# Kernel tuning notes

Hardware: AMD Instinct MI355X
Metric: run time of the kernel (lower is better)

The kernel has to match this reference:

```python
import jax, jax.numpy as jnp
import numpy as np

EMBED = 1024
HEADS = 16
HEAD_DIM = EMBED // HEADS
LN_EPS = 1e-5


def setup_inputs() -> dict:
    key = jax.random.key(0)
    ks = jax.random.split(key, 12)
    B, LQ, LK = 2, 2048, 2048
    s = 1.0 / np.sqrt(EMBED)
    inp = {
        "query_seq": jax.random.normal(ks[0], (B, LQ, EMBED), jnp.float32),
        "key_value_seq": jax.random.normal(ks[1], (B, LK, EMBED), jnp.float32),
        "prompt_size": 0,
        "Wq": jax.random.normal(ks[2], (EMBED, EMBED), jnp.float32) * s,
        "bq": jnp.zeros((EMBED,), jnp.float32),
        "Wk": jax.random.normal(ks[3], (EMBED, EMBED), jnp.float32) * s,
        "bk": jnp.zeros((EMBED,), jnp.float32),
        "Wv": jax.random.normal(ks[4], (EMBED, EMBED), jnp.float32) * s,
        "bv": jnp.zeros((EMBED,), jnp.float32),
        "Wo": jax.random.normal(ks[5], (EMBED, EMBED), jnp.float32) * s,
        "bo": jnp.zeros((EMBED,), jnp.float32),
        "ln_gamma": jnp.ones((EMBED,), jnp.float32),
        "ln_beta": jnp.zeros((EMBED,), jnp.float32),
    }
    return inp


def _split_heads(x):
    B, L, _ = x.shape
    return x.reshape(B, L, HEADS, HEAD_DIM).transpose(0, 2, 1, 3)  # [B,H,L,Dh]


def reference(query_seq, key_value_seq, prompt_size, Wq, bq, Wk, bk, Wv, bv, Wo, bo, ln_gamma, ln_beta):
    # projections (torch nn.Linear: x @ W.T + b)
    q = _split_heads(query_seq @ Wq.T + bq)
    k = _split_heads(key_value_seq @ Wk.T + bk)
    v = _split_heads(key_value_seq @ Wv.T + bv)
    # naive attention: full score matrix, softmax over keys
    scores = jnp.einsum("bhqd,bhkd->bhqk", q, k) / np.sqrt(HEAD_DIM).astype(np.float32)
    attn = jax.nn.softmax(scores, axis=-1)
    ctx = jnp.einsum("bhqk,bhkd->bhqd", attn, v)
    B, H, LQ, Dh = ctx.shape
    ctx = ctx.transpose(0, 2, 1, 3).reshape(B, LQ, H * Dh)
    out = ctx @ Wo.T + bo
    # residual + LayerNorm
    x = out + query_seq
    mu = jnp.mean(x, axis=-1, keepdims=True)
    var = jnp.var(x, axis=-1, keepdims=True)
    return (x - mu) * jax.lax.rsqrt(var + LN_EPS) * ln_gamma + ln_beta
```

## Files before the change

kernel.cpp:

```cpp
#include <hip/hip_runtime.h>

typedef unsigned short u16;
typedef unsigned int u32;
typedef __attribute__((ext_vector_type(8))) __bf16 bf16x8;
typedef __attribute__((ext_vector_type(4))) float f32x4;
typedef __attribute__((ext_vector_type(16))) float f32x16;

#define EMBED 1024
#define NB 2
#define LQ 2048
#define HEADS 16
#define DH 64
#define QSCALE 0.18033688011112042f

__device__ __forceinline__ u16 f2bf(float f) {
  u32 u = __float_as_uint(f);
  u32 r = (u + 0x7FFFu + ((u >> 16) & 1u)) >> 16;
  return (u16)r;
}

__device__ __forceinline__ void glds16(const void* g, void* l) {
  __builtin_amdgcn_global_load_lds((const __attribute__((address_space(1))) void*)g,
                                   (__attribute__((address_space(3))) void*)l, 16, 0, 0);
}

__device__ __forceinline__ f32x4 mfma16(bf16x8 a, bf16x8 b, f32x4 c) {
  return __builtin_amdgcn_mfma_f32_16x16x32_bf16(a, b, c, 0, 0, 0);
}
__device__ __forceinline__ f32x16 mfma32(bf16x8 a, bf16x8 b, f32x16 c) {
  return __builtin_amdgcn_mfma_f32_32x32x16_bf16(a, b, c, 0, 0, 0);
}

__device__ __forceinline__ void pl32(u32& a, u32& b) {
  asm("v_permlane32_swap_b32 %0, %1" : "+v"(a), "+v"(b));
}

__device__ __forceinline__ u32 packbf(float a, float b) {
  return __builtin_amdgcn_perm(__float_as_uint(b), __float_as_uint(a), 0x07060302u);
}

__global__ __launch_bounds__(256) void cast_kernel(
    const float* __restrict__ q, const float* __restrict__ kv,
    const float* __restrict__ wq, const float* __restrict__ wk,
    const float* __restrict__ wv, const float* __restrict__ wo,
    u16* __restrict__ qb, u16* __restrict__ kvb, u16* __restrict__ wqb,
    u16* __restrict__ wkb, u16* __restrict__ wvb, u16* __restrict__ wob) {
  int bid = blockIdx.x;
  const float* src;
  u16* dst;
  long base;
  if (bid < 2048) {
    src = q; dst = qb; base = (long)bid * 2048;
  } else if (bid < 4096) {
    src = kv; dst = kvb; base = (long)(bid - 2048) * 2048;
  } else {
    int wsel = (bid - 4096) >> 9;
    int wb = (bid - 4096) & 511;
    if (wsel == 0) { src = wq; dst = wqb; }
    else if (wsel == 1) { src = wk; dst = wkb; }
    else if (wsel == 2) { src = wv; dst = wvb; }
    else { src = wo; dst = wob; }
    base = (long)wb * 2048;
  }
  long e = base + (long)threadIdx.x * 8;
  float4 f0 = *(const float4*)(src + e);
  float4 f1 = *(const float4*)(src + e + 4);
  uint4 o;
  o.x = (u32)f2bf(f0.x) | ((u32)f2bf(f0.y) << 16);
  o.y = (u32)f2bf(f0.z) | ((u32)f2bf(f0.w) << 16);
  o.z = (u32)f2bf(f1.x) | ((u32)f2bf(f1.y) << 16);
  o.w = (u32)f2bf(f1.z) | ((u32)f2bf(f1.w) << 16);
  *(uint4*)(dst + e) = o;
}

template <int IT>
__device__ __forceinline__ void gemm_core(
    u16* As, u16* Bs, const u16* __restrict__ A, const u16* __restrict__ W,
    const float* __restrict__ bias, const float* __restrict__ resid,
    void* __restrict__ outp, int mode, int bx, int by) {
  const int K = EMBED;
  const int TM = IT * 32;
  const int tid = threadIdx.x;
  const int lane = tid & 63;
  const int wv = tid >> 6;
  const int wm = wv >> 1, wn = wv & 1;
  const int l16 = lane & 15, quad = lane >> 4;
  const long tile_m = (long)bx * TM;
  const long tile_n = (long)by * 128;

  f32x4 z4 = {0.f, 0.f, 0.f, 0.f};
  f32x4 acc[IT][4];
#pragma unroll
  for (int i = 0; i < IT; i++)
#pragma unroll
    for (int j = 0; j < 4; j++) acc[i][j] = z4;

  for (int k0 = 0; k0 < K; k0 += 64) {
#pragma unroll
    for (int it = 0; it < TM / 32; it++) {
      int lin = it * 256 + tid;
      int row = lin >> 3, cc = lin & 7;
      glds16(A + (tile_m + row) * K + k0 + ((cc ^ (row & 7)) << 3), As + lin * 8);
    }
#pragma unroll
    for (int it = 0; it < 4; it++) {
      int lin = it * 256 + tid;
      int row = lin >> 3, cc = lin & 7;
      glds16(W + (tile_n + row) * K + k0 + ((cc ^ (row & 7)) << 3), Bs + lin * 8);
    }
    __syncthreads();
#pragma unroll
    for (int ki = 0; ki < 2; ki++) {
      bf16x8 af[IT], bfr[4];
#pragma unroll
      for (int i = 0; i < IT; i++) {
        int row = wm * (IT * 16) + i * 16 + l16;
        af[i] = *(const bf16x8*)(As + row * 64 + (((ki * 4 + quad) ^ (row & 7)) << 3));
      }
#pragma unroll
      for (int j = 0; j < 4; j++) {
        int row = wn * 64 + j * 16 + l16;
        bfr[j] = *(const bf16x8*)(Bs + row * 64 + (((ki * 4 + quad) ^ (row & 7)) << 3));
      }
#pragma unroll
      for (int i = 0; i < IT; i++)
#pragma unroll
        for (int j = 0; j < 4; j++) acc[i][j] = mfma16(af[i], bfr[j], acc[i][j]);
    }
    __syncthreads();
  }

#pragma unroll
  for (int j = 0; j < 4; j++) {
    int gn = (int)tile_n + wn * 64 + j * 16 + l16;
    float bv = bias[gn];
#pragma unroll
    for (int i = 0; i < IT; i++) {
      long gm0 = tile_m + wm * (IT * 16) + i * 16 + quad * 4;
      if (mode == 3) {
#pragma unroll
        for (int r = 0; r < 4; r++) {
          long idx = (gm0 + r) * EMBED + gn;
          ((float*)outp)[idx] = acc[i][j][r] + bv + resid[idx];
        }
      } else if (mode == 2) {
        int b = (int)(gm0 >> 11), l = (int)(gm0 & 2047);
        int hh = gn >> 6, dh = gn & 63;
        uint2 pk;
        pk.x = (u32)f2bf(acc[i][j][0] + bv) | ((u32)f2bf(acc[i][j][1] + bv) << 16);
        pk.y = (u32)f2bf(acc[i][j][2] + bv) | ((u32)f2bf(acc[i][j][3] + bv) << 16);
        *(uint2*)((u16*)outp + (long)((b * HEADS + hh) * DH + dh) * LQ + l) = pk;
      } else {
#pragma unroll
        for (int r = 0; r < 4; r++) {
          long gm = gm0 + r;
          float v = acc[i][j][r] + bv;
          if (mode == 0) v *= QSCALE;
          int b = (int)(gm >> 11), l = (int)(gm & 2047);
          int hh = gn >> 6, dh = gn & 63;
          ((u16*)outp)[(long)((b * HEADS + hh) * LQ + l) * DH + dh] = f2bf(v);
        }
      }
    }
  }
}

__device__ __forceinline__ void xcd_map(int id, int& bx, int& by) {
  int xcd = id & 7, j = id >> 3;
  bx = (xcd << 3) | (j & 7);
  by = j >> 3;
}

__global__ __launch_bounds__(256, 4) void qkv_kernel(
    const u16* __restrict__ qb, const u16* __restrict__ kvb,
    const u16* __restrict__ wqb, const u16* __restrict__ wkb, const u16* __restrict__ wvb,
    const float* __restrict__ bq, const float* __restrict__ bk, const float* __restrict__ bv,
    u16* __restrict__ Qh, u16* __restrict__ Kh, u16* __restrict__ Vt) {
  __shared__ u16 As[64 * 64];
  __shared__ u16 Bs[128 * 64];
  int bx, by;
  xcd_map((int)blockIdx.x, bx, by);
  int z = blockIdx.y;
  if (z == 0)      gemm_core<2>(As, Bs, qb,  wqb, bq, nullptr, Qh, 0, bx, by);
  else if (z == 1) gemm_core<2>(As, Bs, kvb, wkb, bk, nullptr, Kh, 1, bx, by);
  else             gemm_core<2>(As, Bs, kvb, wvb, bv, nullptr, Vt, 2, bx, by);
}

__global__ __launch_bounds__(256, 4) void oproj_kernel(
    const u16* __restrict__ ctx, const u16* __restrict__ wob,
    const float* __restrict__ bo, const float* __restrict__ resid, float* __restrict__ out) {
  __shared__ u16 As[64 * 64];
  __shared__ u16 Bs[128 * 64];
  int bx, by;
  xcd_map((int)blockIdx.x, bx, by);
  gemm_core<2>(As, Bs, ctx, wob, bo, resid, out, 3, bx, by);
}

__global__ __launch_bounds__(512, 4) void attn_kernel(
    const u16* __restrict__ Qh, const u16* __restrict__ Kh,
    const u16* __restrict__ Vt, u16* __restrict__ ctx) {
  __shared__ u16 KVs[4][2][64 * 64];
  const int tid = threadIdx.x;
  const int lane = tid & 63;
  const int wv = tid >> 6;
  const int qsub = wv >> 1;
  const int kh = wv & 1;
  const int l32 = lane & 31, h = lane >> 5;
  const int bid = (int)blockIdx.x;
  const int swz = (bid & 7) * 64 + (bid >> 3);
  const int bh = swz >> 4, qt = swz & 15;
  const long qoff = (long)bh * (LQ * DH) + (long)qt * (128 * DH);
  const long koff = (long)bh * (LQ * DH);
  const long voff = (long)bh * (DH * LQ);
  const int qbase = qsub * 32;
  const int krow = kh * 32 + l32;

#define STAGE_KV(t, N)                                                          \
  do {                                                                          \
    int row = tid >> 3, cc = tid & 7;                                           \
    glds16(Kh + koff + (long)((t) * 64 + row) * 64 + ((cc ^ (row & 7)) << 3),   \
           &KVs[N][0][0] + tid * 8);                                            \
    glds16(Vt + voff + (long)row * LQ + (t) * 64 + ((cc ^ (row & 7)) << 3),     \
           &KVs[N][1][0] + tid * 8);                                            \
  } while (0)

#define SYNC(W)                                                                 \
  do {                                                                          \
    asm volatile("s_waitcnt vmcnt(" #W ")" ::: "memory");                       \
    __builtin_amdgcn_s_barrier();                                               \
    asm volatile("" ::: "memory");                                              \
  } while (0)

  bf16x8 bq[4];
  {
    const u16* qp = Qh + qoff + (qbase + l32) * 64 + h * 8;
#pragma unroll
    for (int ks = 0; ks < 4; ks++) bq[ks] = *(const bf16x8*)(qp + ks * 16);
  }

  STAGE_KV(0, 0);
  STAGE_KV(1, 1);
  STAGE_KV(2, 2);
  SYNC(2);

  f32x16 z16 = {0.f, 0.f, 0.f, 0.f, 0.f, 0.f, 0.f, 0.f,
                0.f, 0.f, 0.f, 0.f, 0.f, 0.f, 0.f, 0.f};
  f32x16 ot[2];
  ot[0] = z16;
  ot[1] = z16;
  f32x16 st;
  uint2 pk[4];
  float2 ls2 = {0.f, 0.f};

#define DO_S(C)                                                                  \
  do {                                                                           \
    __builtin_amdgcn_s_setprio(1);                                               \
    _Pragma("unroll") for (int ks = 0; ks < 4; ks++) {                           \
      bf16x8 ak = *(const bf16x8*)(&KVs[C][0][0] + krow * 64 +                   \
                                   (((ks * 2 + h) ^ (krow & 7)) << 3));          \
      st = mfma32(ak, bq[ks], (ks == 0) ? z16 : st);                             \
    }                                                                            \
    __builtin_amdgcn_s_setprio(0);                                               \
  } while (0)

#define DO_SM()                                                                  \
  do {                                                                           \
    _Pragma("unroll") for (int g = 0; g < 4; g++) {                              \
      float p0 = __builtin_amdgcn_exp2f(st[g * 4 + 0]);                          \
      float p1 = __builtin_amdgcn_exp2f(st[g * 4 + 1]);                          \
      float p2 = __builtin_amdgcn_exp2f(st[g * 4 + 2]);                          \
      float p3 = __builtin_amdgcn_exp2f(st[g * 4 + 3]);                          \
      ls2.x += p0 + p2;                                                          \
      ls2.y += p1 + p3;                                                          \
      pk[g].x = packbf(p0, p1);                                                  \
      pk[g].y = packbf(p2, p3);                                                  \
    }                                                                            \
  } while (0)

#define DO_PV(P)                                                                 \
  do {                                                                           \
    _Pragma("unroll") for (int s = 0; s < 2; s++) {                              \
      uint2 wa = pk[s * 2];                                                      \
      uint2 wb = pk[s * 2 + 1];                                                  \
      u32 a0 = wa.x, b0 = wb.x, a1 = wa.y, b1 = wb.y;                            \
      pl32(a0, b0);                                                              \
      pl32(a1, b1);                                                              \
      union { u32 u[4]; bf16x8 v; } bp;                                          \
      bp.u[0] = a0;                                                              \
      bp.u[1] = a1;                                                              \
      bp.u[2] = b0;                                                              \
      bp.u[3] = b1;                                                              \
      __builtin_amdgcn_s_setprio(1);                                             \
      _Pragma("unroll") for (int mt2 = 0; mt2 < 2; mt2++) {                      \
        int row = mt2 * 32 + l32;                                                \
        int c = ((2 * kh + s) << 1) + h;                                         \
        bf16x8 av = *(const bf16x8*)(&KVs[P][1][0] + row * 64 +                  \
                                     ((c ^ (row & 7)) << 3));                    \
        ot[mt2] = mfma32(av, bp.v, ot[mt2]);                                     \
      }                                                                          \
      __builtin_amdgcn_s_setprio(0);                                             \
    }                                                                            \
  } while (0)

#define AITER(kt, P, C, N, W)                                                    \
  do {                                                                           \
    if ((kt) + 2 < 32) STAGE_KV((kt) + 2, N);                                    \
    DO_SM();                                                                     \
    DO_S(C);                                                                     \
    DO_PV(P);                                                                    \
    SYNC(W);                                                                     \
  } while (0)

  DO_S(0);

  AITER(1, 0, 1, 3, 2);
  for (int k0 = 2; k0 < 30; k0 += 4) {
    AITER(k0 + 0, 1, 2, 0, 2);
    AITER(k0 + 1, 2, 3, 1, 2);
    AITER(k0 + 2, 3, 0, 2, 2);
    AITER(k0 + 3, 0, 1, 3, 2);
  }
  AITER(30, 1, 2, 0, 0);
  AITER(31, 2, 3, 1, 0);
  DO_SM();
  DO_PV(3);

#undef STAGE_KV
#undef SYNC
#undef DO_S
#undef DO_SM
#undef DO_PV
#undef AITER

  float lsum = ls2.x + ls2.y;
  lsum += __shfl_xor(lsum, 32);

  float* mrgf = (float*)(&KVs[0][0][0]);
  float* mlsf = mrgf + 4 * 64 * 36;
  __syncthreads();
  if (kh == 1) {
    int mbase = (qsub * 64 + lane) * 36;
#pragma unroll
    for (int mt2 = 0; mt2 < 2; mt2++)
#pragma unroll
      for (int e = 0; e < 16; e++) mrgf[mbase + mt2 * 16 + e] = ot[mt2][e];
    mlsf[qsub * 64 + lane] = lsum;
  }
  __syncthreads();
  if (kh == 0) {
    int mbase = (qsub * 64 + lane) * 36;
    lsum += mlsf[qsub * 64 + lane];
    float inv = 1.0f / lsum;
    const int b = bh >> 4, head = bh & 15;
    int qrow = qt * 128 + qbase + l32;
    long base = (long)(b * LQ + qrow) * EMBED + head * DH;
#pragma unroll
    for (int mt2 = 0; mt2 < 2; mt2++) {
#pragma unroll
      for (int g = 0; g < 4; g++) {
        float o0 = (ot[mt2][g * 4 + 0] + mrgf[mbase + mt2 * 16 + g * 4 + 0]) * inv;
        float o1 = (ot[mt2][g * 4 + 1] + mrgf[mbase + mt2 * 16 + g * 4 + 1]) * inv;
        float o2 = (ot[mt2][g * 4 + 2] + mrgf[mbase + mt2 * 16 + g * 4 + 2]) * inv;
        float o3 = (ot[mt2][g * 4 + 3] + mrgf[mbase + mt2 * 16 + g * 4 + 3]) * inv;
        uint2 pkk;
        pkk.x = (u32)f2bf(o0) | ((u32)f2bf(o1) << 16);
        pkk.y = (u32)f2bf(o2) | ((u32)f2bf(o3) << 16);
        *(uint2*)(ctx + base + mt2 * 32 + g * 8 + 4 * h) = pkk;
      }
    }
  }
}

__global__ __launch_bounds__(256) void ln_kernel(
    float* __restrict__ x, const float* __restrict__ gamma, const float* __restrict__ beta) {
  const int lane = threadIdx.x & 63;
  const int wid = threadIdx.x >> 6;
  const long row = (long)blockIdx.x * 4 + wid;
  float* xr = x + row * EMBED;
  float4 v[4];
  float s = 0.f, sq = 0.f;
#pragma unroll
  for (int k = 0; k < 4; k++) {
    v[k] = *(const float4*)(xr + k * 256 + lane * 4);
    s += v[k].x + v[k].y + v[k].z + v[k].w;
    sq += v[k].x * v[k].x + v[k].y * v[k].y + v[k].z * v[k].z + v[k].w * v[k].w;
  }
#pragma unroll
  for (int off = 1; off < 64; off <<= 1) {
    s += __shfl_xor(s, off);
    sq += __shfl_xor(sq, off);
  }
  float mu = s * (1.f / EMBED);
  float var = sq * (1.f / EMBED) - mu * mu;
  float rstd = rsqrtf(var + 1e-5f);
#pragma unroll
  for (int k = 0; k < 4; k++) {
    float4 g = *(const float4*)(gamma + k * 256 + lane * 4);
    float4 bt = *(const float4*)(beta + k * 256 + lane * 4);
    float4 ov;
    ov.x = (v[k].x - mu) * rstd * g.x + bt.x;
    ov.y = (v[k].y - mu) * rstd * g.y + bt.y;
    ov.z = (v[k].z - mu) * rstd * g.z + bt.z;
    ov.w = (v[k].w - mu) * rstd * g.w + bt.w;
    *(float4*)(xr + k * 256 + lane * 4) = ov;
  }
}

extern "C" void kernel_launch(void* const* d_in, const int* in_sizes, int n_in,
                              void* d_out, int out_size, void* d_ws, size_t ws_size,
                              hipStream_t stream) {
  const float* q     = (const float*)d_in[0];
  const float* kv    = (const float*)d_in[1];
  const float* Wq    = (const float*)d_in[3];
  const float* bq    = (const float*)d_in[4];
  const float* Wk    = (const float*)d_in[5];
  const float* bk    = (const float*)d_in[6];
  const float* Wv    = (const float*)d_in[7];
  const float* bv    = (const float*)d_in[8];
  const float* Wo    = (const float*)d_in[9];
  const float* bo    = (const float*)d_in[10];
  const float* gamma = (const float*)d_in[11];
  const float* beta  = (const float*)d_in[12];

  char* ws = (char*)d_ws;
  u16* qb  = (u16*)(ws + (0l  << 20));
  u16* kvb = (u16*)(ws + (8l  << 20));
  u16* wqb = (u16*)(ws + (16l << 20));
  u16* wkb = (u16*)(ws + (18l << 20));
  u16* wvb = (u16*)(ws + (20l << 20));
  u16* wob = (u16*)(ws + (22l << 20));
  u16* Qh  = (u16*)(ws + (24l << 20));
  u16* Kh  = (u16*)(ws + (32l << 20));
  u16* Vt  = (u16*)(ws + (40l << 20));
  u16* ctx = (u16*)(ws + (48l << 20));
  float* out = (float*)d_out;

  cast_kernel<<<6144, 256, 0, stream>>>(q, kv, Wq, Wk, Wv, Wo, qb, kvb, wqb, wkb, wvb, wob);
  qkv_kernel<<<dim3(512, 3), 256, 0, stream>>>(qb, kvb, wqb, wkb, wvb, bq, bk, bv, Qh, Kh, Vt);
  attn_kernel<<<512, 512, 0, stream>>>(Qh, Kh, Vt, ctx);
  oproj_kernel<<<512, 256, 0, stream>>>(ctx, wob, bo, q, out);
  ln_kernel<<<1024, 256, 0, stream>>>(out, gamma, beta);
}
```

Measured before the change: 207.5 us.

## Fuse K and V projections into one GEMM block sharing the A tile

Adds a kv_core routine that computes the K and V projections together in each block. It loads the key/value activation tile once into LDS and reuses it against both Wk and Wv tiles, which halves the A-operand traffic for those two GEMMs. The qkv launch drops from 3 to 2 grid rows. In exchange, each block needs twice the B-tile LDS and twice the accumulator registers, and the kernel becomes imbalanced: the K/V blocks do double the work of the Q blocks.

New measurement: 203.4 us. 1.02x faster.

```diff
diff --git a/kernel.cpp b/kernel.cpp
--- a/kernel.cpp
+++ b/kernel.cpp
@@ -165,6 +165,100 @@
   }
 }
 
+__device__ __forceinline__ void kv_core(
+    u16* As, u16* Bk, u16* Bv,
+    const u16* __restrict__ A, const u16* __restrict__ Wk, const u16* __restrict__ Wv,
+    const float* __restrict__ bkb, const float* __restrict__ bvb,
+    u16* __restrict__ Kh, u16* __restrict__ Vt, int bx, int by) {
+  const int K = EMBED;
+  const int tid = threadIdx.x;
+  const int lane = tid & 63;
+  const int wvv = tid >> 6;
+  const int wm = wvv >> 1, wn = wvv & 1;
+  const int l16 = lane & 15, quad = lane >> 4;
+  const long tile_m = (long)bx * 64;
+  const long tile_n = (long)by * 128;
+
+  f32x4 z4 = {0.f, 0.f, 0.f, 0.f};
+  f32x4 accK[2][4], accV[2][4];
+#pragma unroll
+  for (int i = 0; i < 2; i++)
+#pragma unroll
+    for (int j = 0; j < 4; j++) { accK[i][j] = z4; accV[i][j] = z4; }
+
+  for (int k0 = 0; k0 < K; k0 += 64) {
+#pragma unroll
+    for (int it = 0; it < 2; it++) {
+      int lin = it * 256 + tid;
+      int row = lin >> 3, cc = lin & 7;
+      glds16(A + (tile_m + row) * K + k0 + ((cc ^ (row & 7)) << 3), As + lin * 8);
+    }
+#pragma unroll
+    for (int it = 0; it < 4; it++) {
+      int lin = it * 256 + tid;
+      int row = lin >> 3, cc = lin & 7;
+      glds16(Wk + (tile_n + row) * K + k0 + ((cc ^ (row & 7)) << 3), Bk + lin * 8);
+      glds16(Wv + (tile_n + row) * K + k0 + ((cc ^ (row & 7)) << 3), Bv + lin * 8);
+    }
+    __syncthreads();
+#pragma unroll
+    for (int ki = 0; ki < 2; ki++) {
+      bf16x8 af[2];
+#pragma unroll
+      for (int i = 0; i < 2; i++) {
+        int row = wm * 32 + i * 16 + l16;
+        af[i] = *(const bf16x8*)(As + row * 64 + (((ki * 4 + quad) ^ (row & 7)) << 3));
+      }
+      {
+        bf16x8 bf[4];
+#pragma unroll
+        for (int j = 0; j < 4; j++) {
+          int row = wn * 64 + j * 16 + l16;
+          bf[j] = *(const bf16x8*)(Bk + row * 64 + (((ki * 4 + quad) ^ (row & 7)) << 3));
+        }
+#pragma unroll
+        for (int i = 0; i < 2; i++)
+#pragma unroll
+          for (int j = 0; j < 4; j++) accK[i][j] = mfma16(af[i], bf[j], accK[i][j]);
+      }
+      {
+        bf16x8 bf[4];
+#pragma unroll
+        for (int j = 0; j < 4; j++) {
+          int row = wn * 64 + j * 16 + l16;
+          bf[j] = *(const bf16x8*)(Bv + row * 64 + (((ki * 4 + quad) ^ (row & 7)) << 3));
+        }
+#pragma unroll
+        for (int i = 0; i < 2; i++)
+#pragma unroll
+          for (int j = 0; j < 4; j++) accV[i][j] = mfma16(af[i], bf[j], accV[i][j]);
+      }
+    }
+    __syncthreads();
+  }
+
+#pragma unroll
+  for (int j = 0; j < 4; j++) {
+    int gn = (int)tile_n + wn * 64 + j * 16 + l16;
+    float bK = bkb[gn];
+    float bV = bvb[gn];
+    int hh = gn >> 6, dh = gn & 63;
+#pragma unroll
+    for (int i = 0; i < 2; i++) {
+      long gm0 = tile_m + wm * 32 + i * 16 + quad * 4;
+      int b = (int)(gm0 >> 11), l0 = (int)(gm0 & 2047);
+#pragma unroll
+      for (int r = 0; r < 4; r++) {
+        Kh[(long)((b * HEADS + hh) * LQ + (l0 + r)) * DH + dh] = f2bf(accK[i][j][r] + bK);
+      }
+      uint2 pk;
+      pk.x = (u32)f2bf(accV[i][j][0] + bV) | ((u32)f2bf(accV[i][j][1] + bV) << 16);
+      pk.y = (u32)f2bf(accV[i][j][2] + bV) | ((u32)f2bf(accV[i][j][3] + bV) << 16);
+      *(uint2*)(Vt + (long)((b * HEADS + hh) * DH + dh) * LQ + l0) = pk;
+    }
+  }
+}
+
 __device__ __forceinline__ void xcd_map(int id, int& bx, int& by) {
   int xcd = id & 7, j = id >> 3;
   bx = (xcd << 3) | (j & 7);
@@ -177,13 +271,13 @@
     const float* __restrict__ bq, const float* __restrict__ bk, const float* __restrict__ bv,
     u16* __restrict__ Qh, u16* __restrict__ Kh, u16* __restrict__ Vt) {
   __shared__ u16 As[64 * 64];
-  __shared__ u16 Bs[128 * 64];
+  __shared__ u16 Bs[2][128 * 64];
   int bx, by;
   xcd_map((int)blockIdx.x, bx, by);
-  int z = blockIdx.y;
-  if (z == 0)      gemm_core<2>(As, Bs, qb,  wqb, bq, nullptr, Qh, 0, bx, by);
-  else if (z == 1) gemm_core<2>(As, Bs, kvb, wkb, bk, nullptr, Kh, 1, bx, by);
-  else             gemm_core<2>(As, Bs, kvb, wvb, bv, nullptr, Vt, 2, bx, by);
+  if (blockIdx.y == 0)
+    gemm_core<2>(As, Bs[0], qb, wqb, bq, nullptr, Qh, 0, bx, by);
+  else
+    kv_core(As, Bs[0], Bs[1], kvb, wkb, wvb, bk, bv, Kh, Vt, bx, by);
 }
 
 __global__ __launch_bounds__(256, 4) void oproj_kernel(
@@ -436,7 +530,7 @@
   float* out = (float*)d_out;
 
   cast_kernel<<<6144, 256, 0, stream>>>(q, kv, Wq, Wk, Wv, Wo, qb, kvb, wqb, wkb, wvb, wob);
-  qkv_kernel<<<dim3(512, 3), 256, 0, stream>>>(qb, kvb, wqb, wkb, wvb, bq, bk, bv, Qh, Kh, Vt);
+  qkv_kernel<<<dim3(512, 2), 256, 0, stream>>>(qb, kvb, wqb, wkb, wvb, bq, bk, bv, Qh, Kh, Vt);
   attn_kernel<<<512, 512, 0, stream>>>(Qh, Kh, Vt, ctx);
   oproj_kernel<<<512, 256, 0, stream>>>(ctx, wob, bo, q, out);
   ln_kernel<<<1024, 256, 0, stream>>>(out, gamma, beta);
```
